# Optimization experiments

Measured on AMD Instinct MI355X. Metric: run time of the kernel, lower is better.

## Reference

```python
import jax, jax.numpy as jnp
import numpy as np

N, E, Z, C, B, G, T = 10000, 160000, 10, 64, 8, 16, 2
R_MAX = 5.0
AVG_NEIGH = 16.0
L_SLICES = ((0, 1), (1, 4), (4, 9))  # l=0,1,2 blocks of the 9 SH components


def sph_harm(u):
    # component-normalized real spherical harmonics up to l=2, u: [E,3] unit vectors
    x, y, z = u[:, 0], u[:, 1], u[:, 2]
    s3, s5, s15 = 3.0 ** 0.5, 5.0 ** 0.5, 15.0 ** 0.5
    return jnp.stack([
        jnp.ones_like(x),
        s3 * x, s3 * y, s3 * z,
        s15 * x * y, s15 * y * z, (s5 / 2) * (3 * z * z - 1), s15 * x * z, (s15 / 2) * (x * x - y * y),
    ], axis=1)  # [E,9]


def radial_embed(r):
    # Bessel basis * polynomial cutoff (p=5), r: [E]
    u = r / R_MAX
    n = jnp.arange(1, B + 1, dtype=jnp.float32)
    bessel = jnp.sqrt(2.0 / R_MAX) * jnp.sin(n[None, :] * jnp.pi * u[:, None]) / (r[:, None] + 1e-9)
    p = 5.0
    fc = 1 - (p + 1) * (p + 2) / 2 * u ** p + p * (p + 2) * u ** (p + 1) - p * (p + 1) / 2 * u ** (p + 2)
    fc = jnp.where(u < 1.0, fc, 0.0)
    return bessel * fc[:, None]  # [E,B]


def per_l_linear(x, W):
    # x: [n,C,9], W: [3,C,C]; independent channel mixing per l-block
    return jnp.concatenate([
        jnp.einsum('ncm,cd->ndm', x[:, :, s:e], W[l]) for l, (s, e) in enumerate(L_SLICES)
    ], axis=2)


def _forward(positions, node_attrs, charges, shifts, W_emb, atomic_energies,
             W_r1, W_r2, W_mix, W_sc, w_poly, W_prod, w_e, w_d,
             edge_index, batch, num_graphs):
    sender, receiver = edge_index[0], edge_index[1]
    # atomic reference energies
    node_e0 = node_attrs @ atomic_energies  # [N]
    e0 = jax.ops.segment_sum(node_e0, batch, num_segments=num_graphs)
    # node embedding: scalars only
    node_feats = jnp.zeros((positions.shape[0], C, 9), positions.dtype)
    node_feats = node_feats.at[:, :, 0].set(node_attrs @ W_emb)
    # edge geometry
    vec = positions[sender] - positions[receiver] + shifts  # [E,3]
    lengths = jnp.sqrt(jnp.sum(vec * vec, axis=1) + 1e-12)
    sh = sph_harm(vec / lengths[:, None])        # [E,9]
    edge_feats = radial_embed(lengths)           # [E,B]
    energies = [e0]
    dipoles = []
    for t in range(T):
        # radial MLP -> per-channel TP weights
        w = jax.nn.silu(edge_feats @ W_r1[t]) @ W_r2[t]      # [E,C]
        h_s = node_feats[sender, :, 0]                       # gather sender scalars [E,C]
        m = (w * h_s)[:, :, None] * sh[:, None, :]           # TP message [E,C,9]
        agg = jax.ops.segment_sum(m, receiver, num_segments=positions.shape[0]) / AVG_NEIGH
        msg = per_l_linear(agg, W_mix[t])
        sc = per_l_linear(node_feats, W_sc[t])               # self-connection
        # product basis (correlation 3): channel-wise scalar polynomial gate
        s0 = msg[:, :, 0]
        poly = w_poly[t, :, 0][None] + w_poly[t, :, 1][None] * s0 + w_poly[t, :, 2][None] * s0 * s0
        node_feats = per_l_linear(msg * poly[:, :, None], W_prod[t]) + sc
        # readout: 1x0e energy + 1x1o dipole
        e_n = node_feats[:, :, 0] @ w_e[t]                   # [N]
        energies.append(jax.ops.segment_sum(e_n, batch, num_segments=num_graphs))
        dipoles.append(jnp.einsum('ncm,c->nm', node_feats[:, :, 1:4], w_d[t]))  # [N,3]
    contributions = jnp.stack(energies, axis=-1)             # [G,T+1]
    total_energy = jnp.sum(contributions, axis=-1)           # [G]
    atomic_dipoles = jnp.sum(jnp.stack(dipoles, axis=-1), axis=-1)  # [N,3]
    total_dipole = jax.ops.segment_sum(atomic_dipoles, batch, num_segments=num_graphs)
    total_dipole = total_dipole + jax.ops.segment_sum(charges[:, None] * positions, batch, num_segments=num_graphs)
    return total_energy, contributions, atomic_dipoles, total_dipole


def setup_inputs():
    key = jax.random.key(0)
    ks = jax.random.split(key, 16)
    s = 0.1
    species = jax.random.randint(ks[1], (N,), 0, Z)
    return {
        'positions': jax.random.normal(ks[0], (N, 3)) * 3.0,
        'node_attrs': jax.nn.one_hot(species, Z, dtype=jnp.float32),
        'charges': jax.random.normal(ks[2], (N,)) * 0.1,
        'shifts': jnp.zeros((E, 3), jnp.float32),
        'W_emb': jax.random.normal(ks[5], (Z, C)) * s,
        'atomic_energies': jax.random.normal(ks[6], (Z,)) * s,
        'W_r1': jax.random.normal(ks[7], (T, B, 64)) * s,
        'W_r2': jax.random.normal(ks[8], (T, 64, C)) * s,
        'W_mix': jax.random.normal(ks[9], (T, 3, C, C)) * s,
        'W_sc': jax.random.normal(ks[10], (T, 3, C, C)) * s,
        'w_poly': jax.random.normal(ks[11], (T, C, 3)) * s,
        'W_prod': jax.random.normal(ks[12], (T, 3, C, C)) * s,
        'w_e': jax.random.normal(ks[13], (T, C)) * s,
        'w_d': jax.random.normal(ks[14], (T, C)) * s,
        'edge_index': jax.random.randint(ks[3], (2, E), 0, N),
        'batch': jnp.sort(jax.random.randint(ks[4], (N,), 0, G)),
        'num_graphs': G,
    }


def reference(positions, node_attrs, charges, shifts, W_emb, atomic_energies,
              W_r1, W_r2, W_mix, W_sc, w_poly, W_prod, w_e, w_d,
              edge_index, batch, num_graphs):
    args = (node_attrs, charges, shifts, W_emb, atomic_energies, W_r1, W_r2,
            W_mix, W_sc, w_poly, W_prod, w_e, w_d, edge_index, batch, num_graphs)
    total_energy, contributions, atomic_dipoles, total_dipole = _forward(positions, *args)
    forces = -jax.grad(lambda p: jnp.sum(_forward(p, *args)[0]))(positions)
    return total_energy, contributions, forces, total_dipole, atomic_dipoles
```

## Files before the change

### kernel.cpp

```cpp
#include <hip/hip_runtime.h>
#include <hip/hip_bf16.h>

#define NN 10000
#define NE 160000
#define NZ 10
#define NBES 8
#define NG 16
#define NT 2
#define NB 2048
#define NB1 2049
#define PL ((size_t)NN*64)

static constexpr float PI_F  = 3.14159265358979323846f;
static constexpr float KBES  = 0.63245553203367587f;
static constexpr float S3    = 1.73205080756887729f;

static constexpr size_t OFF_UVL  = 0;
static constexpr size_t OFF_PIN  = OFF_UVL + (size_t)NE*4;
static constexpr size_t OFF_ATT  = OFF_PIN + (size_t)NN*3;
static constexpr size_t OFF_CHG  = OFF_ATT + (size_t)NN*NZ;
static constexpr size_t OFF_SHF  = OFF_CHG + (size_t)NN;
static constexpr size_t OFF_NF0  = OFF_SHF + (size_t)NE*3;
static constexpr size_t OFF_NF1  = OFF_NF0 + PL;
static constexpr size_t OFF_MSG0 = OFF_NF1 + 4*PL;
static constexpr size_t OFF_MSG1 = OFF_MSG0 + 4*PL;
static constexpr size_t OFF_AGG  = OFF_MSG1 + 4*PL;
static constexpr size_t O_GA1    = OFF_MSG0 + PL;
static constexpr size_t O_GA0    = OFF_AGG;
static constexpr size_t OFF_W    = OFF_AGG + 4*PL;
static constexpr size_t O_WEMB   = OFF_W;
static constexpr size_t O_AE     = O_WEMB + 640;
static constexpr size_t O_R1     = O_AE   + 16;
static constexpr size_t O_R2     = O_R1   + 1024;
static constexpr size_t O_WMIX   = O_R2   + 8192;
static constexpr size_t O_WMIXT  = O_WMIX + 24576;
static constexpr size_t O_WSC    = O_WMIXT+ 24576;
static constexpr size_t O_WSCT   = O_WSC  + 24576;
static constexpr size_t O_WPROD  = O_WSCT + 24576;
static constexpr size_t O_WPRODT = O_WPROD+ 24576;
static constexpr size_t O_WPOLY  = O_WPRODT+24576;
static constexpr size_t O_WE     = O_WPOLY+ 384;
static constexpr size_t O_WD     = O_WE   + 128;
static constexpr size_t OFF_ACC  = O_WD   + 128;
static constexpr size_t O_E0G    = OFF_ACC;
static constexpr size_t O_ETG    = O_E0G + 16;
static constexpr size_t O_TD     = O_ETG + 32;
static constexpr size_t O_ADP    = O_TD  + 48;
static constexpr size_t O_GPOS   = O_ADP + (size_t)NN*3;
static constexpr size_t ACC_FLOATS = 96 + (size_t)NN*6;
static constexpr size_t O_EN0    = O_GPOS + (size_t)NN*3;
static constexpr size_t O_EN1    = O_EN0 + NN;
static constexpr size_t O_E0N    = O_EN1 + NN;
static constexpr size_t O_FLAG   = O_E0N + NN;
static constexpr size_t O_TW     = O_FLAG + 4;
static constexpr size_t O_TQ     = O_TW + (size_t)2*NB1*64;
static constexpr size_t O_OFFR   = O_TQ + (size_t)2*NB1*64;
static constexpr size_t O_OFFS   = O_OFFR + (NN+1);
static constexpr size_t O_CURR   = O_OFFS + (NN+1);
static constexpr size_t O_CURS   = O_CURR + NN;
static constexpr size_t O_RECRAW = O_CURS + NN;
static constexpr size_t O_RECR   = (O_RECRAW + 7) & ~(size_t)7;
static constexpr size_t O_RECS   = O_RECR + (size_t)NE*8 + 64;
static constexpr size_t WS_FLOATS= O_RECS + (size_t)NE*8 + 64;

__device__ __forceinline__ float rlane(float v, int l){
  return __int_as_float(__builtin_amdgcn_readlane(__float_as_int(v), l));
}
__device__ __forceinline__ int irlane(float v, int l){
  return __builtin_amdgcn_readlane(__float_as_int(v), l);
}

static constexpr int LD_CNT[14] = {NN*3, NN*NZ, NN, NE*3, NZ*64, NZ, NT*NBES*64, NT*64*64,
                                   NT*3*64*64, NT*3*64*64, NT*64*3, NT*3*64*64, NT*64, NT*64};
static constexpr int LD_TOTAL = NN*3 + NN*NZ + NN + NE*3 + NZ*64 + NZ + NT*NBES*64 + NT*64*64
                              + 3*(NT*3*64*64) + NT*64*3 + 4*(NT*64) - NT*64*2;
__global__ __launch_bounds__(256) void k_load_all(
    const void* s0, const void* s1, const void* s2, const void* s3, const void* s4,
    const void* s5, const void* s6, const void* s7, const void* s8, const void* s9,
    const void* s10, const void* s11, const void* s12, const void* s13,
    float* __restrict__ ws){
  __shared__ int found;
  if (threadIdx.x == 0) found = 0;
  __syncthreads();
  const unsigned* raw = (const unsigned*)s1;
  int f = 0;
  for (int i = threadIdx.x; i < 4096; i += 256){
    unsigned w = raw[i];
    f |= (w == 0x00003F80u || w == 0x3F803F80u) ? 1 : 0;
  }
  if (f) found = 1;
  __syncthreads();
  const int isbf = found;
  if (blockIdx.x == 0 && threadIdx.x == 0) ((int*)(ws + O_FLAG))[0] = isbf;

  const void* srcs[14] = {s0,s1,s2,s3,s4,s5,s6,s7,s8,s9,s10,s11,s12,s13};
  const size_t dsts[14] = {OFF_PIN, OFF_ATT, OFF_CHG, OFF_SHF, O_WEMB, O_AE, O_R1, O_R2,
                           O_WMIX, O_WSC, O_WPOLY, O_WPROD, O_WE, O_WD};
  int i = blockIdx.x*256 + threadIdx.x;
  int seg = -1, off = i;
  #pragma unroll
  for (int j = 0; j < 14; ++j){
    if (seg < 0){
      if (off < LD_CNT[j]) seg = j;
      else off -= LD_CNT[j];
    }
  }
  if (seg < 0) return;
  float v = isbf ? __bfloat162float(((const __hip_bfloat16*)srcs[seg])[off])
                 : ((const float*)srcs[seg])[off];
  ws[dsts[seg] + off] = v;
}

static constexpr int GEOM_B = (NE+255)/256;
static constexpr int TAB_B  = (2*NB1+3)/4;
static constexpr int INIT_B = (NN+3)/4;
static constexpr int TRAN_B = 5*4096/256;
__global__ __launch_bounds__(256, 3) void k_prep(float* __restrict__ ws, const int* __restrict__ ei){
  int b = blockIdx.x;
  if (b < GEOM_B){
    int e = b*256 + threadIdx.x;
    if (e >= NE) return;
    const float* pos = ws + OFF_PIN;
    const float* shifts = ws + OFF_SHF;
    int s = ei[e], r = ei[NE + e];
    float vx = pos[s*3+0] - pos[r*3+0] + shifts[(size_t)e*3+0];
    float vy = pos[s*3+1] - pos[r*3+1] + shifts[(size_t)e*3+1];
    float vz = pos[s*3+2] - pos[r*3+2] + shifts[(size_t)e*3+2];
    float L = sqrtf(vx*vx + vy*vy + vz*vz + 1e-12f);
    float inv = 1.f / L;
    float4 uq; uq.x = vx*inv; uq.y = vy*inv; uq.z = vz*inv; uq.w = L;
    *(float4*)(ws + OFF_UVL + (size_t)e*4) = uq;
    if (L < 5.f){
      atomicAdd((int*)(ws + O_CURR) + r, 1);
      atomicAdd((int*)(ws + O_CURS) + s, 1);
    }
  } else if (b < GEOM_B + TAB_B){
    int lane = threadIdx.x & 63;
    int task = (b - GEOM_B)*4 + (threadIdx.x >> 6);
    if (task >= 2*NB1) return;
    int t = task / NB1, node = task % NB1;
    const float* R1 = ws + O_R1 + (size_t)t*512;
    const float* R2 = ws + O_R2 + (size_t)t*4096;
    float r1c[8];
    #pragma unroll
    for (int j = 0; j < 8; ++j) r1c[j] = R1[j*64 + lane];
    float L = fmaxf((float)node * (5.f/NB), 1e-6f);
    float ur = L*0.2f;
    float ef[8], dd[8];
    if (ur < 1.f){
      float u2=ur*ur, u4=u2*u2, u5=u4*ur;
      float fc = 1.f - 21.f*u5 + 35.f*u5*ur - 15.f*u5*u2;
      float omu = 1.f - ur;
      float dfc = -105.f*u4*omu*omu;
      float invr = 1.f/(L + 1e-9f);
      #pragma unroll
      for (int bb = 0; bb < 8; ++bb){
        float nb = (float)(bb+1);
        float arg = nb*PI_F*ur;
        float sn = __sinf(arg), cs = __cosf(arg);
        float bes = KBES*sn*invr;
        float dbes = KBES*(nb*PI_F*0.2f)*cs*invr - bes*invr;
        ef[bb] = bes*fc;
        dd[bb] = dbes*fc + bes*dfc*0.2f;
      }
    } else {
      #pragma unroll
      for (int bb = 0; bb < 8; ++bb){ ef[bb] = 0.f; dd[bb] = 0.f; }
    }
    float a = 0.f, tt = 0.f;
    #pragma unroll
    for (int bb = 0; bb < 8; ++bb){ a = fmaf(ef[bb], r1c[bb], a); tt = fmaf(r1c[bb], dd[bb], tt); }
    float sg = 1.f/(1.f + __expf(-a));
    float sl = a*sg;
    float q  = sg*fmaf(a, 1.f - sg, 1.f)*tt;
    float r2c[64];
    #pragma unroll
    for (int j = 0; j < 64; ++j) r2c[j] = R2[j*64 + lane];
    float W0=0.f, W1=0.f, Q0=0.f, Q1=0.f;
    #pragma unroll
    for (int j = 0; j < 64; j += 2){
      W0 = fmaf(rlane(sl, j  ), r2c[j  ], W0);
      W1 = fmaf(rlane(sl, j+1), r2c[j+1], W1);
      Q0 = fmaf(rlane(q,  j  ), r2c[j  ], Q0);
      Q1 = fmaf(rlane(q,  j+1), r2c[j+1], Q1);
    }
    size_t idx = ((size_t)t*NB1 + node)*64 + lane;
    ws[O_TW + idx] = (W0+W1)*(1.f/16.f);
    ws[O_TQ + idx] = (Q0+Q1)*(1.f/16.f);
  } else if (b < GEOM_B + TAB_B + INIT_B){
    int lane = threadIdx.x & 63;
    int n = (b - GEOM_B - TAB_B)*4 + (threadIdx.x >> 6);
    if (n >= NN) return;
    const float* attrs = ws + OFF_ATT;
    float acc = 0.f;
    #pragma unroll
    for (int z = 0; z < NZ; ++z) acc = fmaf(attrs[(size_t)n*NZ+z], ws[O_WEMB + z*64 + lane], acc);
    ws[OFF_NF0 + (size_t)n*64 + lane] = acc;
    if (lane == 0){
      float e = 0.f;
      #pragma unroll
      for (int z = 0; z < NZ; ++z) e = fmaf(attrs[(size_t)n*NZ+z], ws[O_AE + z], e);
      ws[O_E0N + n] = e;
    }
  } else {
    int i = (b - GEOM_B - TAB_B - INIT_B)*256 + threadIdx.x;
    int mat = i >> 12, r = (i >> 6) & 63, c = i & 63;
    const size_t src[5] = {O_WMIX, O_WMIX+12288, O_WPROD, O_WPROD+12288, O_WSC+12288};
    const size_t dst[5] = {O_WMIXT, O_WMIXT+12288, O_WPRODT, O_WPRODT+12288, O_WSCT+12288};
    ws[dst[mat] + (size_t)c*64 + r] = ws[src[mat] + (size_t)r*64 + c];
  }
}

__global__ __launch_bounds__(1024) void k_csr_scan(
    int* __restrict__ curr, int* __restrict__ curs,
    int* __restrict__ offr, int* __restrict__ offs_){
  __shared__ unsigned short cr[NN], cs[NN];
  __shared__ int pr[1024], ps[1024];
  int tid = threadIdx.x;
  for (int i = tid; i < NN; i += 1024){
    cr[i] = (unsigned short)curr[i];
    cs[i] = (unsigned short)curs[i];
  }
  __syncthreads();
  const int chunk = (NN + 1023)/1024;
  int lo = tid*chunk, hi = lo + chunk;
  if (hi > NN) hi = NN;
  if (lo > NN) lo = NN;
  int sr = 0, ss = 0;
  for (int i = lo; i < hi; ++i){ sr += cr[i]; ss += cs[i]; }
  pr[tid] = sr; ps[tid] = ss;
  __syncthreads();
  for (int o = 1; o < 1024; o <<= 1){
    int vr = (tid >= o) ? pr[tid-o] : 0;
    int vs = (tid >= o) ? ps[tid-o] : 0;
    __syncthreads();
    pr[tid] += vr; ps[tid] += vs;
    __syncthreads();
  }
  int runr = tid ? pr[tid-1] : 0;
  int runs = tid ? ps[tid-1] : 0;
  for (int i = lo; i < hi; ++i){
    int a = cr[i], c = cs[i];
    offr[i] = runr; curr[i] = runr; runr += a;
    offs_[i] = runs; curs[i] = runs; runs += c;
  }
  if (tid == 1023){ offr[NN] = runr; offs_[NN] = runs; }
}

__global__ void k_csr_fill(const int* __restrict__ ei, const float* __restrict__ uvl,
                           int* __restrict__ curr, int* __restrict__ curs,
                           float* __restrict__ recr, float* __restrict__ recs){
  int e = blockIdx.x*256 + threadIdx.x;
  if (e >= NE) return;
  float4 q = *(const float4*)(uvl + (size_t)e*4);
  if (q.w >= 5.f) return;
  int s = ei[e], r = ei[NE + e];
  int4 meta; meta.x = s; meta.y = r; meta.z = e; meta.w = 0;
  int pr = atomicAdd(&curr[r], 1);
  *(float4*)(recr + (size_t)pr*8) = q;
  *(int4*)(recr + (size_t)pr*8 + 4) = meta;
  int ps = atomicAdd(&curs[s], 1);
  *(float4*)(recs + (size_t)ps*8) = q;
  *(int4*)(recs + (size_t)ps*8 + 4) = meta;
}

__global__ __launch_bounds__(256) void k_agg(
    const float* __restrict__ TWt, const float* __restrict__ recr,
    const float* __restrict__ h, const int* __restrict__ offr,
    float* __restrict__ agg){
  int lane = threadIdx.x & 63;
  int wid = blockIdx.x*4 + (threadIdx.x >> 6);
  int nw  = gridDim.x*4;
  for (int n = wid; n < NN; n += nw){
    int lo = offr[n], hi = offr[n+1];
    float c0=0.f, x1=0.f, y1=0.f, z1=0.f;
    for (int i = lo; i < hi; i += 8){
      float rv = recr[(size_t)i*8 + lane];
      int cnt = hi - i;
      if (cnt >= 8){
        #pragma unroll
        for (int j = 0; j < 8; ++j){
          float ux = rlane(rv, j*8+0), uy = rlane(rv, j*8+1), uz = rlane(rv, j*8+2);
          float L  = rlane(rv, j*8+3);
          int   s  = irlane(rv, j*8+4);
          float pos = L*(NB/5.f); int bi = (int)pos; float f = pos - (float)bi;
          const float* T = TWt + (size_t)bi*64 + lane;
          float t0 = T[0];
          float w = fmaf(T[64]-t0, f, t0);
          float wh = w * h[(size_t)s*64 + lane];
          c0 += wh;
          x1 = fmaf(wh, ux, x1);
          y1 = fmaf(wh, uy, y1);
          z1 = fmaf(wh, uz, z1);
        }
      } else {
        for (int j = 0; j < cnt; ++j){
          float ux = rlane(rv, j*8+0), uy = rlane(rv, j*8+1), uz = rlane(rv, j*8+2);
          float L  = rlane(rv, j*8+3);
          int   s  = irlane(rv, j*8+4);
          float pos = L*(NB/5.f); int bi = (int)pos; float f = pos - (float)bi;
          const float* T = TWt + (size_t)bi*64 + lane;
          float t0 = T[0];
          float w = fmaf(T[64]-t0, f, t0);
          float wh = w * h[(size_t)s*64 + lane];
          c0 += wh;
          x1 = fmaf(wh, ux, x1);
          y1 = fmaf(wh, uy, y1);
          z1 = fmaf(wh, uz, z1);
        }
      }
    }
    size_t ob = (size_t)n*64 + lane;
    agg[ob]        = c0;
    agg[ob+PL]     = S3*x1;
    agg[ob+2*PL]   = S3*y1;
    agg[ob+3*PL]   = S3*z1;
  }
}

template<int GB1>
__global__ __launch_bounds__(256, 3) void k_lin2(
    const float* __restrict__ in, const float* __restrict__ W3, float* __restrict__ out,
    const float* __restrict__ WMIXT1, const float* __restrict__ WPRODT1,
    const float* __restrict__ we1, const float* __restrict__ wp1,
    float* __restrict__ ga1){
  int k = blockIdx.y;
  int l = (k==0) ? 0 : 1;
  const float* W = W3 + (size_t)l*4096;
  int lane = threadIdx.x & 63;
  float wcol[64];
  #pragma unroll
  for (int j = 0; j < 64; ++j) wcol[j] = W[j*64 + lane];
  float wcol2[64];
  float g = 0.f, p0 = 0.f, p1 = 0.f, p2 = 0.f;
  const bool gb1 = GB1 && (k == 0);
  if (gb1){
    #pragma unroll
    for (int j = 0; j < 64; ++j) wcol2[j] = WMIXT1[j*64 + lane];
    #pragma unroll
    for (int c = 0; c < 64; ++c) g = fmaf(we1[c], WPRODT1[c*64 + lane], g);
    p0 = wp1[lane*3]; p1 = wp1[lane*3+1]; p2 = wp1[lane*3+2];
  }
  int wid = blockIdx.x*4 + (threadIdx.x >> 6);
  int nw  = gridDim.x*4;
  const float* inp = in + (size_t)k*PL;
  float* outp = out + (size_t)k*PL;
  for (int n = wid; n < NN; n += nw){
    float x = inp[(size_t)n*64 + lane];
    float a0 = 0.f, a1 = 0.f, a2 = 0.f, a3 = 0.f;
    #pragma unroll
    for (int j = 0; j < 64; j += 4){
      a0 = fmaf(rlane(x, j  ), wcol[j  ], a0);
      a1 = fmaf(rlane(x, j+1), wcol[j+1], a1);
      a2 = fmaf(rlane(x, j+2), wcol[j+2], a2);
      a3 = fmaf(rlane(x, j+3), wcol[j+3], a3);
    }
    float m = (a0+a1) + (a2+a3);
    outp[(size_t)n*64 + lane] = m;
    if (gb1){
      float poly = fmaf(fmaf(p2, m, p1), m, p0);
      float dp   = fmaf(2.f*p2, m, p1);
      float gb = g*fmaf(m, dp, poly);
      float b0=0.f, b1=0.f, b2=0.f, b3=0.f;
      #pragma unroll
      for (int j = 0; j < 64; j += 4){
        b0 = fmaf(rlane(gb, j  ), wcol2[j  ], b0);
        b1 = fmaf(rlane(gb, j+1), wcol2[j+1], b1);
        b2 = fmaf(rlane(gb, j+2), wcol2[j+2], b2);
        b3 = fmaf(rlane(gb, j+3), wcol2[j+3], b3);
      }
      ga1[(size_t)n*64 + lane] = (b0+b1) + (b2+b3);
    }
  }
}

template<int WRITE_NF, int NF_SINGLE>
__global__ __launch_bounds__(256, 3) void k_tail(
    const float* __restrict__ nf_in, const float* __restrict__ msg,
    const float* __restrict__ Wsc, const float* __restrict__ Wprod, const float* __restrict__ wp,
    const float* __restrict__ we, const float* __restrict__ wd,
    float* __restrict__ nf_out, float* __restrict__ en, float* __restrict__ adp){
  int lane = threadIdx.x & 63;
  int k = threadIdx.x >> 6;
  int l = (k==0) ? 0 : 1;
  const bool use_sc = !(NF_SINGLE && k > 0);
  float wcs[64], wcp[64];
  #pragma unroll
  for (int j = 0; j < 64; ++j)
    wcp[j] = Wprod[(size_t)l*4096 + j*64 + lane];
  if (use_sc){
    #pragma unroll
    for (int j = 0; j < 64; ++j)
      wcs[j] = Wsc[(size_t)l*4096 + j*64 + lane];
  }
  float p0 = wp[lane*3], p1 = wp[lane*3+1], p2 = wp[lane*3+2];
  float rw = (k==0) ? we[lane] : wd[lane];
  const float* msgk = msg + (size_t)k*PL;
  const float* nfk  = nf_in + (size_t)k*PL;
  float* outk = nf_out + (size_t)k*PL;
  for (int n = blockIdx.x; n < NN; n += gridDim.x){
    size_t base = (size_t)n*64 + lane;
    float s0 = msg[base];
    float xm = (k==0) ? s0 : msgk[base];
    float xg = xm * fmaf(fmaf(p2, s0, p1), s0, p0);
    float b0=0.f, b1=0.f;
    #pragma unroll
    for (int j = 0; j < 64; j += 2){
      b0 = fmaf(rlane(xg, j  ), wcp[j  ], b0);
      b1 = fmaf(rlane(xg, j+1), wcp[j+1], b1);
    }
    float out = b0 + b1;
    if (use_sc){
      float xs = nfk[base];
      float a0=0.f, a1=0.f;
      #pragma unroll
      for (int j = 0; j < 64; j += 2){
        a0 = fmaf(rlane(xs, j  ), wcs[j  ], a0);
        a1 = fmaf(rlane(xs, j+1), wcs[j+1], a1);
      }
      out += a0 + a1;
    }
    if (WRITE_NF) outk[base] = out;
    float red = out * rw;
    #pragma unroll
    for (int o = 32; o; o >>= 1) red += __shfl_xor(red, o, 64);
    if (lane == 0){
      if (k == 0) en[n] = red;
      else        adp[n*3 + (k-1)] += red;
    }
  }
}

static constexpr int GHG_GRID = 1024;
static constexpr int RED_B = (NN+255)/256;
__global__ __launch_bounds__(256) void k_ghg0(float* __restrict__ ws, const int* __restrict__ offs_,
                                              const int* __restrict__ batch){
  __shared__ float wl[2*4096];
  if (blockIdx.x >= GHG_GRID){
    int n = (blockIdx.x - GHG_GRID)*256 + threadIdx.x;
    int lane = threadIdx.x & 63;
    bool valid = (n < NN);
    int g = valid ? batch[n] : -1;
    float v0=0.f, v1=0.f, v2=0.f, tx=0.f, ty=0.f, tz=0.f;
    if (valid){
      v0 = ws[O_E0N + n]; v1 = ws[O_EN0 + n]; v2 = ws[O_EN1 + n];
      float qq = ws[OFF_CHG + n];
      tx = ws[O_ADP + n*3+0] + qq*ws[OFF_PIN + n*3+0];
      ty = ws[O_ADP + n*3+1] + qq*ws[OFF_PIN + n*3+1];
      tz = ws[O_ADP + n*3+2] + qq*ws[OFF_PIN + n*3+2];
    }
    float* e0g = ws + O_E0G; float* Etg = ws + O_ETG; float* td = ws + O_TD;
    int g0 = __shfl(g, 0, 64), g63 = __shfl(g, 63, 64);
    if (g0 == g63 && g0 >= 0){
      #pragma unroll
      for (int o = 32; o; o >>= 1){
        v0 += __shfl_xor(v0, o, 64); v1 += __shfl_xor(v1, o, 64); v2 += __shfl_xor(v2, o, 64);
        tx += __shfl_xor(tx, o, 64); ty += __shfl_xor(ty, o, 64); tz += __shfl_xor(tz, o, 64);
      }
      if (lane == 0){
        atomicAdd(&e0g[g0], v0); atomicAdd(&Etg[g0], v1); atomicAdd(&Etg[16+g0], v2);
        atomicAdd(&td[g0*3+0], tx); atomicAdd(&td[g0*3+1], ty); atomicAdd(&td[g0*3+2], tz);
      }
    } else if (valid){
      atomicAdd(&e0g[g], v0); atomicAdd(&Etg[g], v1); atomicAdd(&Etg[16+g], v2);
      atomicAdd(&td[g*3+0], tx); atomicAdd(&td[g*3+1], ty); atomicAdd(&td[g*3+2], tz);
    }
    return;
  }
  for (int i = threadIdx.x; i < 4096; i += 256){
    wl[i]        = ws[O_WPRODT + i];
    wl[4096 + i] = ws[O_WMIXT + i];
  }
  __syncthreads();
  const int lane = threadIdx.x & 63;
  int wid = blockIdx.x*4 + (threadIdx.x >> 6);
  const int nw = GHG_GRID*4;
  float gnfc = ws[O_WE + lane];
  {
    const float* WS1 = ws + O_WSCT + 12288;
    const float* we1 = ws + O_WE + 64;
    #pragma unroll
    for (int c = 0; c < 64; ++c) gnfc = fmaf(we1[c], WS1[c*64 + lane], gnfc);
  }
  const float p0 = ws[O_WPOLY + lane*3];
  const float p1 = ws[O_WPOLY + lane*3 + 1];
  const float p2 = ws[O_WPOLY + lane*3 + 2];
  const float* TW1 = ws + O_TW + (size_t)NB1*64;
  const float* recs = ws + O_RECS;
  const float* GA1 = ws + O_GA1;
  for (int n = wid; n < NN; n += nw){
    int lo = offs_[n], hi = offs_[n+1];
    float acc = 0.f;
    for (int i = lo; i < hi; i += 8){
      float rv = recs[(size_t)i*8 + lane];
      int cnt = hi - i;
      if (cnt >= 8){
        #pragma unroll
        for (int j = 0; j < 8; ++j){
          float L = rlane(rv, j*8+3);
          int   r = irlane(rv, j*8+5);
          float pos = L*(NB/5.f); int bi = (int)pos; float f = pos - (float)bi;
          const float* T = TW1 + (size_t)bi*64 + lane;
          float t0 = T[0];
          float w = fmaf(T[64]-t0, f, t0);
          acc = fmaf(w, GA1[(size_t)r*64 + lane], acc);
        }
      } else {
        for (int j = 0; j < cnt; ++j){
          float L = rlane(rv, j*8+3);
          int   r = irlane(rv, j*8+5);
          float pos = L*(NB/5.f); int bi = (int)pos; float f = pos - (float)bi;
          const float* T = TW1 + (size_t)bi*64 + lane;
          float t0 = T[0];
          float w = fmaf(T[64]-t0, f, t0);
          acc = fmaf(w, GA1[(size_t)r*64 + lane], acc);
        }
      }
    }
    float gB = gnfc + acc;
    float q0=0.f, q1=0.f;
    #pragma unroll
    for (int j = 0; j < 64; j += 2){
      q0 = fmaf(rlane(gB,j),   wl[j*64 + lane],     q0);
      q1 = fmaf(rlane(gB,j+1), wl[(j+1)*64 + lane], q1);
    }
    float gmp = q0 + q1;
    float s0v = ws[OFF_MSG0 + (size_t)n*64 + lane];
    float poly = fmaf(fmaf(p2, s0v, p1), s0v, p0);
    float dp   = fmaf(2.f*p2, s0v, p1);
    float gb = gmp * fmaf(s0v, dp, poly);
    float u0=0.f, u1=0.f;
    #pragma unroll
    for (int j = 0; j < 64; j += 2){
      u0 = fmaf(rlane(gb,j),   wl[4096 + j*64 + lane],     u0);
      u1 = fmaf(rlane(gb,j+1), wl[4096 + (j+1)*64 + lane], u1);
    }
    ws[O_GA0 + (size_t)n*64 + lane] = u0 + u1;
  }
}

__global__ __launch_bounds__(256) void k_bwdE2(float* __restrict__ ws, const int* __restrict__ nlive_ptr){
  const int lane = threadIdx.x & 63;
  int wid = blockIdx.x*4 + (threadIdx.x >> 6);
  const int nw = gridDim.x*4;
  const int nlive = nlive_ptr[0];
  const int ngrp = (nlive + 7) >> 3;
  const float* recs = ws + O_RECS;
  const float* TQ  = ws + O_TQ;
  const float* h0  = ws + OFF_NF0;
  const float* h1  = ws + OFF_NF1;
  const float* ga0 = ws + O_GA0;
  const float* ga1 = ws + O_GA1;
  float* gpos = ws + O_GPOS;
  for (int gi = wid; gi < ngrp; gi += nw){
    const int i0 = gi*8;
    float rv = recs[(size_t)i0*8 + lane];
    int cnt = nlive - i0; if (cnt > 8) cnt = 8;
    #pragma unroll 8
    for (int j = 0; j < cnt; ++j){
      float ux = rlane(rv, j*8+0), uy = rlane(rv, j*8+1), uz = rlane(rv, j*8+2);
      float L  = rlane(rv, j*8+3);
      int   s  = irlane(rv, j*8+4);
      int   r  = irlane(rv, j*8+5);
      float pos = L*(NB/5.f); int bi = (int)pos; float f = pos - (float)bi;
      const float* T0 = TQ + (size_t)bi*64 + lane;
      const float* T1 = T0 + (size_t)NB1*64;
      float Q0 = fmaf(T0[64]-T0[0], f, T0[0]);
      float Q1 = fmaf(T1[64]-T1[0], f, T1[0]);
      float rr = Q0*h0[(size_t)s*64 + lane]*ga0[(size_t)r*64 + lane]
               + Q1*h1[(size_t)s*64 + lane]*ga1[(size_t)r*64 + lane];
      #pragma unroll
      for (int o = 32; o; o >>= 1) rr += __shfl_xor(rr, o, 64);
      if (lane < 3){
        float u = (lane==0) ? ux : ((lane==1) ? uy : uz);
        float v = rr*u;
        atomicAdd(&gpos[(size_t)s*3 + lane],  v);
        atomicAdd(&gpos[(size_t)r*3 + lane], -v);
      }
    }
  }
}

__global__ void k_writeout(const float* __restrict__ e0g, const float* __restrict__ Etg,
                           const float* __restrict__ td, const float* __restrict__ adp,
                           const float* __restrict__ gpos, void* __restrict__ outv,
                           const int* __restrict__ flag){
  int i = blockIdx.x*256 + threadIdx.x;
  const int total = NG + NG*3 + NN*3 + NG*3 + NN*3;
  if (i >= total) return;
  float v;
  if (i < 16){
    v = e0g[i] + Etg[i] + Etg[16+i];
  } else if (i < 64){
    int j = i - 16; int g = j/3, t = j - g*3;
    v = (t == 0) ? e0g[g] : Etg[(t-1)*16 + g];
  } else if (i < 64 + NN*3){
    v = -gpos[i-64];
  } else if (i < 64 + NN*3 + 48){
    v = td[i - (64 + NN*3)];
  } else {
    v = adp[i - (64 + NN*3 + 48)];
  }
  if (flag[0]) ((__hip_bfloat16*)outv)[i] = __float2bfloat16(v);
  else         ((float*)outv)[i] = v;
}

extern "C" void kernel_launch(void* const* d_in, const int* in_sizes, int n_in,
                              void* d_out, int out_size, void* d_ws, size_t ws_size,
                              hipStream_t stream) {
  if (ws_size < WS_FLOATS*sizeof(float)) return;
  const int* ei    = (const int*)d_in[14];
  const int* batch = (const int*)d_in[15];
  float* ws = (float*)d_ws;

  int* offr  = (int*)(ws + O_OFFR);
  int* offs_ = (int*)(ws + O_OFFS);
  int* curr  = (int*)(ws + O_CURR);
  int* curs  = (int*)(ws + O_CURS);

  hipMemsetAsync(ws + OFF_ACC, 0, ACC_FLOATS*sizeof(float), stream);
  hipMemsetAsync(curr, 0, 2*NN*sizeof(int), stream);

  k_load_all<<<(LD_TOTAL+255)/256, 256, 0, stream>>>(
      d_in[0], d_in[1], d_in[2], d_in[3], d_in[4], d_in[5], d_in[6], d_in[7],
      d_in[8], d_in[9], d_in[10], d_in[11], d_in[12], d_in[13], ws);
  k_prep<<<GEOM_B + TAB_B + INIT_B + TRAN_B, 256, 0, stream>>>(ws, ei);
  k_csr_scan<<<1, 1024, 0, stream>>>(curr, curs, offr, offs_);
  k_csr_fill<<<(NE+255)/256, 256, 0, stream>>>(ei, ws+OFF_UVL, curr, curs,
                                               ws+O_RECR, ws+O_RECS);

  dim3 ling(256, 4);

  k_agg<<<1024, 256, 0, stream>>>(ws+O_TW, ws+O_RECR, ws+OFF_NF0, offr, ws+OFF_AGG);
  k_lin2<0><<<ling, 256, 0, stream>>>(ws+OFF_AGG, ws+O_WMIX, ws+OFF_MSG0,
                                      ws, ws, ws, ws, ws);
  k_tail<1,1><<<1024, 256, 0, stream>>>(ws+OFF_NF0, ws+OFF_MSG0,
                                        ws+O_WSC, ws+O_WPROD,
                                        ws+O_WPOLY, ws+O_WE, ws+O_WD,
                                        ws+OFF_NF1, ws+O_EN0, ws+O_ADP);
  k_agg<<<1024, 256, 0, stream>>>(ws+O_TW + (size_t)NB1*64, ws+O_RECR, ws+OFF_NF1, offr, ws+OFF_AGG);
  k_lin2<1><<<ling, 256, 0, stream>>>(ws+OFF_AGG, ws+O_WMIX + 12288, ws+OFF_MSG1,
                                      ws+O_WMIXT + 12288, ws+O_WPRODT + 12288,
                                      ws+O_WE + 64, ws+O_WPOLY + 192, ws+O_GA1);
  k_tail<0,0><<<1024, 256, 0, stream>>>(ws+OFF_NF1, ws+OFF_MSG1,
                                        ws+O_WSC + 12288, ws+O_WPROD + 12288,
                                        ws+O_WPOLY + 192, ws+O_WE + 64, ws+O_WD + 64,
                                        ws+OFF_NF1, ws+O_EN1, ws+O_ADP);

  k_ghg0<<<GHG_GRID + RED_B, 256, 0, stream>>>(ws, offs_, batch);
  k_bwdE2<<<2048, 256, 0, stream>>>(ws, offs_ + NN);

  k_writeout<<<(60112+255)/256, 256, 0, stream>>>(ws+O_E0G, ws+O_ETG, ws+O_TD, ws+O_ADP,
                                                  ws+O_GPOS, d_out, (const int*)(ws+O_FLAG));
}
```

Measured before the change: 332.4 us.

## Interleave radial table neighbors as float2, prefetch edge records, move weights to registers

The radial weight tables are stored interleaved so each lane fetches both interpolation endpoints in a single float2 load, where before it issued two separate scalar loads. The edge-record loops in k_agg and k_ghg0 now prefetch the next group of 8 records while the current group is processed. k_ghg0 keeps its two 64x64 weight columns in registers instead of shared memory, and launch bounds are added to several kernels. In exchange the tables take twice the memory and register pressure rises, which could cause spills or lower occupancy.

```diff
diff --git a/kernel.cpp b/kernel.cpp
--- a/kernel.cpp
+++ b/kernel.cpp
@@ -53,8 +53,8 @@
 static constexpr size_t O_E0N    = O_EN1 + NN;
 static constexpr size_t O_FLAG   = O_E0N + NN;
 static constexpr size_t O_TW     = O_FLAG + 4;
-static constexpr size_t O_TQ     = O_TW + (size_t)2*NB1*64;
-static constexpr size_t O_OFFR   = O_TQ + (size_t)2*NB1*64;
+static constexpr size_t O_TQ     = O_TW + (size_t)2*NB1*128;
+static constexpr size_t O_OFFR   = O_TQ + (size_t)2*NB1*128;
 static constexpr size_t O_OFFS   = O_OFFR + (NN+1);
 static constexpr size_t O_CURR   = O_OFFS + (NN+1);
 static constexpr size_t O_CURS   = O_CURR + NN;
@@ -184,9 +184,15 @@
       Q0 = fmaf(rlane(q,  j  ), r2c[j  ], Q0);
       Q1 = fmaf(rlane(q,  j+1), r2c[j+1], Q1);
     }
-    size_t idx = ((size_t)t*NB1 + node)*64 + lane;
-    ws[O_TW + idx] = (W0+W1)*(1.f/16.f);
-    ws[O_TQ + idx] = (Q0+Q1)*(1.f/16.f);
+    float Wv = (W0+W1)*(1.f/16.f);
+    float Qv = (Q0+Q1)*(1.f/16.f);
+    size_t base2 = ((size_t)t*NB1 + node)*128 + (size_t)lane*2;
+    ws[O_TW + base2] = Wv;
+    ws[O_TQ + base2] = Qv;
+    if (node > 0){
+      ws[O_TW + base2 - 128 + 1] = Wv;
+      ws[O_TQ + base2 - 128 + 1] = Qv;
+    }
   } else if (b < GEOM_B + TAB_B + INIT_B){
     int lane = threadIdx.x & 63;
     int n = (b - GEOM_B - TAB_B)*4 + (threadIdx.x >> 6);
@@ -264,7 +270,7 @@
   *(int4*)(recs + (size_t)ps*8 + 4) = meta;
 }
 
-__global__ __launch_bounds__(256) void k_agg(
+__global__ __launch_bounds__(256, 4) void k_agg(
     const float* __restrict__ TWt, const float* __restrict__ recr,
     const float* __restrict__ h, const int* __restrict__ offr,
     float* __restrict__ agg){
@@ -274,40 +280,43 @@
   for (int n = wid; n < NN; n += nw){
     int lo = offr[n], hi = offr[n+1];
     float c0=0.f, x1=0.f, y1=0.f, z1=0.f;
-    for (int i = lo; i < hi; i += 8){
-      float rv = recr[(size_t)i*8 + lane];
-      int cnt = hi - i;
-      if (cnt >= 8){
-        #pragma unroll
-        for (int j = 0; j < 8; ++j){
-          float ux = rlane(rv, j*8+0), uy = rlane(rv, j*8+1), uz = rlane(rv, j*8+2);
-          float L  = rlane(rv, j*8+3);
-          int   s  = irlane(rv, j*8+4);
-          float pos = L*(NB/5.f); int bi = (int)pos; float f = pos - (float)bi;
-          const float* T = TWt + (size_t)bi*64 + lane;
-          float t0 = T[0];
-          float w = fmaf(T[64]-t0, f, t0);
-          float wh = w * h[(size_t)s*64 + lane];
-          c0 += wh;
-          x1 = fmaf(wh, ux, x1);
-          y1 = fmaf(wh, uy, y1);
-          z1 = fmaf(wh, uz, z1);
+    if (lo < hi){
+      float rv = recr[(size_t)lo*8 + lane];
+      for (int i = lo; i < hi; ){
+        int ni = i + 8;
+        float rvn = (ni < hi) ? recr[(size_t)ni*8 + lane] : 0.f;
+        int cnt = hi - i;
+        if (cnt >= 8){
+          #pragma unroll
+          for (int j = 0; j < 8; ++j){
+            float ux = rlane(rv, j*8+0), uy = rlane(rv, j*8+1), uz = rlane(rv, j*8+2);
+            float L  = rlane(rv, j*8+3);
+            int   s  = irlane(rv, j*8+4);
+            float pos = L*(NB/5.f); int bi = (int)pos; float f = pos - (float)bi;
+            const float2 tp = *(const float2*)(TWt + ((size_t)bi*64 + lane)*2);
+            float w = fmaf(tp.y - tp.x, f, tp.x);
+            float wh = w * h[(size_t)s*64 + lane];
+            c0 += wh;
+            x1 = fmaf(wh, ux, x1);
+            y1 = fmaf(wh, uy, y1);
+            z1 = fmaf(wh, uz, z1);
+          }
+        } else {
+          for (int j = 0; j < cnt; ++j){
+            float ux = rlane(rv, j*8+0), uy = rlane(rv, j*8+1), uz = rlane(rv, j*8+2);
+            float L  = rlane(rv, j*8+3);
+            int   s  = irlane(rv, j*8+4);
+            float pos = L*(NB/5.f); int bi = (int)pos; float f = pos - (float)bi;
+            const float2 tp = *(const float2*)(TWt + ((size_t)bi*64 + lane)*2);
+            float w = fmaf(tp.y - tp.x, f, tp.x);
+            float wh = w * h[(size_t)s*64 + lane];
+            c0 += wh;
+            x1 = fmaf(wh, ux, x1);
+            y1 = fmaf(wh, uy, y1);
+            z1 = fmaf(wh, uz, z1);
+          }
         }
-      } else {
-        for (int j = 0; j < cnt; ++j){
-          float ux = rlane(rv, j*8+0), uy = rlane(rv, j*8+1), uz = rlane(rv, j*8+2);
-          float L  = rlane(rv, j*8+3);
-          int   s  = irlane(rv, j*8+4);
-          float pos = L*(NB/5.f); int bi = (int)pos; float f = pos - (float)bi;
-          const float* T = TWt + (size_t)bi*64 + lane;
-          float t0 = T[0];
-          float w = fmaf(T[64]-t0, f, t0);
-          float wh = w * h[(size_t)s*64 + lane];
-          c0 += wh;
-          x1 = fmaf(wh, ux, x1);
-          y1 = fmaf(wh, uy, y1);
-          z1 = fmaf(wh, uz, z1);
-        }
+        rv = rvn; i = ni;
       }
     }
     size_t ob = (size_t)n*64 + lane;
@@ -433,9 +442,8 @@
 
 static constexpr int GHG_GRID = 1024;
 static constexpr int RED_B = (NN+255)/256;
-__global__ __launch_bounds__(256) void k_ghg0(float* __restrict__ ws, const int* __restrict__ offs_,
-                                              const int* __restrict__ batch){
-  __shared__ float wl[2*4096];
+__global__ __launch_bounds__(256, 2) void k_ghg0(float* __restrict__ ws, const int* __restrict__ offs_,
+                                                 const int* __restrict__ batch){
   if (blockIdx.x >= GHG_GRID){
     int n = (blockIdx.x - GHG_GRID)*256 + threadIdx.x;
     int lane = threadIdx.x & 63;
@@ -467,12 +475,12 @@
     }
     return;
   }
-  for (int i = threadIdx.x; i < 4096; i += 256){
-    wl[i]        = ws[O_WPRODT + i];
-    wl[4096 + i] = ws[O_WMIXT + i];
-  }
-  __syncthreads();
   const int lane = threadIdx.x & 63;
+  float wcp[64], wcm[64];
+  #pragma unroll
+  for (int j = 0; j < 64; ++j) wcp[j] = ws[O_WPRODT + j*64 + lane];
+  #pragma unroll
+  for (int j = 0; j < 64; ++j) wcm[j] = ws[O_WMIXT + j*64 + lane];
   int wid = blockIdx.x*4 + (threadIdx.x >> 6);
   const int nw = GHG_GRID*4;
   float gnfc = ws[O_WE + lane];
@@ -485,44 +493,47 @@
   const float p0 = ws[O_WPOLY + lane*3];
   const float p1 = ws[O_WPOLY + lane*3 + 1];
   const float p2 = ws[O_WPOLY + lane*3 + 2];
-  const float* TW1 = ws + O_TW + (size_t)NB1*64;
+  const float* TW1 = ws + O_TW + (size_t)NB1*128;
   const float* recs = ws + O_RECS;
   const float* GA1 = ws + O_GA1;
   for (int n = wid; n < NN; n += nw){
     int lo = offs_[n], hi = offs_[n+1];
     float acc = 0.f;
-    for (int i = lo; i < hi; i += 8){
-      float rv = recs[(size_t)i*8 + lane];
-      int cnt = hi - i;
-      if (cnt >= 8){
-        #pragma unroll
-        for (int j = 0; j < 8; ++j){
-          float L = rlane(rv, j*8+3);
-          int   r = irlane(rv, j*8+5);
-          float pos = L*(NB/5.f); int bi = (int)pos; float f = pos - (float)bi;
-          const float* T = TW1 + (size_t)bi*64 + lane;
-          float t0 = T[0];
-          float w = fmaf(T[64]-t0, f, t0);
-          acc = fmaf(w, GA1[(size_t)r*64 + lane], acc);
+    if (lo < hi){
+      float rv = recs[(size_t)lo*8 + lane];
+      for (int i = lo; i < hi; ){
+        int ni = i + 8;
+        float rvn = (ni < hi) ? recs[(size_t)ni*8 + lane] : 0.f;
+        int cnt = hi - i;
+        if (cnt >= 8){
+          #pragma unroll
+          for (int j = 0; j < 8; ++j){
+            float L = rlane(rv, j*8+3);
+            int   r = irlane(rv, j*8+5);
+            float pos = L*(NB/5.f); int bi = (int)pos; float f = pos - (float)bi;
+            const float2 tp = *(const float2*)(TW1 + ((size_t)bi*64 + lane)*2);
+            float w = fmaf(tp.y - tp.x, f, tp.x);
+            acc = fmaf(w, GA1[(size_t)r*64 + lane], acc);
+          }
+        } else {
+          for (int j = 0; j < cnt; ++j){
+            float L = rlane(rv, j*8+3);
+            int   r = irlane(rv, j*8+5);
+            float pos = L*(NB/5.f); int bi = (int)pos; float f = pos - (float)bi;
+            const float2 tp = *(const float2*)(TW1 + ((size_t)bi*64 + lane)*2);
+            float w = fmaf(tp.y - tp.x, f, tp.x);
+            acc = fmaf(w, GA1[(size_t)r*64 + lane], acc);
+          }
         }
-      } else {
-        for (int j = 0; j < cnt; ++j){
-          float L = rlane(rv, j*8+3);
-          int   r = irlane(rv, j*8+5);
-          float pos = L*(NB/5.f); int bi = (int)pos; float f = pos - (float)bi;
-          const float* T = TW1 + (size_t)bi*64 + lane;
-          float t0 = T[0];
-          float w = fmaf(T[64]-t0, f, t0);
-          acc = fmaf(w, GA1[(size_t)r*64 + lane], acc);
-        }
+        rv = rvn; i = ni;
       }
     }
     float gB = gnfc + acc;
     float q0=0.f, q1=0.f;
     #pragma unroll
     for (int j = 0; j < 64; j += 2){
-      q0 = fmaf(rlane(gB,j),   wl[j*64 + lane],     q0);
-      q1 = fmaf(rlane(gB,j+1), wl[(j+1)*64 + lane], q1);
+      q0 = fmaf(rlane(gB,j),   wcp[j  ], q0);
+      q1 = fmaf(rlane(gB,j+1), wcp[j+1], q1);
     }
     float gmp = q0 + q1;
     float s0v = ws[OFF_MSG0 + (size_t)n*64 + lane];
@@ -532,21 +543,22 @@
     float u0=0.f, u1=0.f;
     #pragma unroll
     for (int j = 0; j < 64; j += 2){
-      u0 = fmaf(rlane(gb,j),   wl[4096 + j*64 + lane],     u0);
-      u1 = fmaf(rlane(gb,j+1), wl[4096 + (j+1)*64 + lane], u1);
+      u0 = fmaf(rlane(gb,j),   wcm[j  ], u0);
+      u1 = fmaf(rlane(gb,j+1), wcm[j+1], u1);
     }
     ws[O_GA0 + (size_t)n*64 + lane] = u0 + u1;
   }
 }
 
-__global__ __launch_bounds__(256) void k_bwdE2(float* __restrict__ ws, const int* __restrict__ nlive_ptr){
+__global__ __launch_bounds__(256, 4) void k_bwdE2(float* __restrict__ ws, const int* __restrict__ nlive_ptr){
   const int lane = threadIdx.x & 63;
   int wid = blockIdx.x*4 + (threadIdx.x >> 6);
   const int nw = gridDim.x*4;
   const int nlive = nlive_ptr[0];
   const int ngrp = (nlive + 7) >> 3;
   const float* recs = ws + O_RECS;
-  const float* TQ  = ws + O_TQ;
+  const float* TQ0 = ws + O_TQ;
+  const float* TQ1 = ws + O_TQ + (size_t)NB1*128;
   const float* h0  = ws + OFF_NF0;
   const float* h1  = ws + OFF_NF1;
   const float* ga0 = ws + O_GA0;
@@ -563,10 +575,10 @@
       int   s  = irlane(rv, j*8+4);
       int   r  = irlane(rv, j*8+5);
       float pos = L*(NB/5.f); int bi = (int)pos; float f = pos - (float)bi;
-      const float* T0 = TQ + (size_t)bi*64 + lane;
-      const float* T1 = T0 + (size_t)NB1*64;
-      float Q0 = fmaf(T0[64]-T0[0], f, T0[0]);
-      float Q1 = fmaf(T1[64]-T1[0], f, T1[0]);
+      const float2 t0 = *(const float2*)(TQ0 + ((size_t)bi*64 + lane)*2);
+      const float2 t1 = *(const float2*)(TQ1 + ((size_t)bi*64 + lane)*2);
+      float Q0 = fmaf(t0.y - t0.x, f, t0.x);
+      float Q1 = fmaf(t1.y - t1.x, f, t1.x);
       float rr = Q0*h0[(size_t)s*64 + lane]*ga0[(size_t)r*64 + lane]
                + Q1*h1[(size_t)s*64 + lane]*ga1[(size_t)r*64 + lane];
       #pragma unroll
@@ -638,7 +650,7 @@
                                         ws+O_WSC, ws+O_WPROD,
                                         ws+O_WPOLY, ws+O_WE, ws+O_WD,
                                         ws+OFF_NF1, ws+O_EN0, ws+O_ADP);
-  k_agg<<<1024, 256, 0, stream>>>(ws+O_TW + (size_t)NB1*64, ws+O_RECR, ws+OFF_NF1, offr, ws+OFF_AGG);
+  k_agg<<<1024, 256, 0, stream>>>(ws+O_TW + (size_t)NB1*128, ws+O_RECR, ws+OFF_NF1, offr, ws+OFF_AGG);
   k_lin2<1><<<ling, 256, 0, stream>>>(ws+OFF_AGG, ws+O_WMIX + 12288, ws+OFF_MSG1,
                                       ws+O_WMIXT + 12288, ws+O_WPRODT + 12288,
                                       ws+O_WE + 64, ws+O_WPOLY + 192, ws+O_GA1);
```

Measured after the change: 335.0 us. Within noise of the previous version (+0.8%).

## Move layer-1 edge position-gradient term into k_ghg0 as extra blocks

Applied to the files above, without the earlier changes.

The layer-1 contribution to the edge force accumulation (using h1, ga1 and the second radial table) is split out of k_bwdE2 and computed by extra blocks appended to the k_ghg0 launch. This lets it overlap with the ghg0 work, since it depends only on data that is ready before that kernel, and it shortens the k_bwdE2 critical path. In exchange the edge records are read twice and the atomics to gpos are doubled, which adds memory traffic and atomic contention.

```diff
diff --git a/kernel.cpp b/kernel.cpp
--- a/kernel.cpp
+++ b/kernel.cpp
@@ -433,9 +433,47 @@
 
 static constexpr int GHG_GRID = 1024;
 static constexpr int RED_B = (NN+255)/256;
+static constexpr int EDGE1_B = 1024;
 __global__ __launch_bounds__(256) void k_ghg0(float* __restrict__ ws, const int* __restrict__ offs_,
                                               const int* __restrict__ batch){
   __shared__ float wl[2*4096];
+  if (blockIdx.x >= GHG_GRID + RED_B){
+    const int lane = threadIdx.x & 63;
+    int wid = (blockIdx.x - GHG_GRID - RED_B)*4 + (threadIdx.x >> 6);
+    const int nw = EDGE1_B*4;
+    const int nlive = offs_[NN];
+    const int ngrp = (nlive + 7) >> 3;
+    const float* recs = ws + O_RECS;
+    const float* TQ1 = ws + O_TQ + (size_t)NB1*64;
+    const float* h1  = ws + OFF_NF1;
+    const float* ga1 = ws + O_GA1;
+    float* gpos = ws + O_GPOS;
+    for (int gi = wid; gi < ngrp; gi += nw){
+      const int i0 = gi*8;
+      float rv = recs[(size_t)i0*8 + lane];
+      int cnt = nlive - i0; if (cnt > 8) cnt = 8;
+      #pragma unroll 8
+      for (int j = 0; j < cnt; ++j){
+        float ux = rlane(rv, j*8+0), uy = rlane(rv, j*8+1), uz = rlane(rv, j*8+2);
+        float L  = rlane(rv, j*8+3);
+        int   s  = irlane(rv, j*8+4);
+        int   r  = irlane(rv, j*8+5);
+        float pos = L*(NB/5.f); int bi = (int)pos; float f = pos - (float)bi;
+        const float* T1 = TQ1 + (size_t)bi*64 + lane;
+        float Q1 = fmaf(T1[64]-T1[0], f, T1[0]);
+        float rr = Q1*h1[(size_t)s*64 + lane]*ga1[(size_t)r*64 + lane];
+        #pragma unroll
+        for (int o = 32; o; o >>= 1) rr += __shfl_xor(rr, o, 64);
+        if (lane < 3){
+          float u = (lane==0) ? ux : ((lane==1) ? uy : uz);
+          float v = rr*u;
+          atomicAdd(&gpos[(size_t)s*3 + lane],  v);
+          atomicAdd(&gpos[(size_t)r*3 + lane], -v);
+        }
+      }
+    }
+    return;
+  }
   if (blockIdx.x >= GHG_GRID){
     int n = (blockIdx.x - GHG_GRID)*256 + threadIdx.x;
     int lane = threadIdx.x & 63;
@@ -548,9 +586,7 @@
   const float* recs = ws + O_RECS;
   const float* TQ  = ws + O_TQ;
   const float* h0  = ws + OFF_NF0;
-  const float* h1  = ws + OFF_NF1;
   const float* ga0 = ws + O_GA0;
-  const float* ga1 = ws + O_GA1;
   float* gpos = ws + O_GPOS;
   for (int gi = wid; gi < ngrp; gi += nw){
     const int i0 = gi*8;
@@ -564,11 +600,8 @@
       int   r  = irlane(rv, j*8+5);
       float pos = L*(NB/5.f); int bi = (int)pos; float f = pos - (float)bi;
       const float* T0 = TQ + (size_t)bi*64 + lane;
-      const float* T1 = T0 + (size_t)NB1*64;
       float Q0 = fmaf(T0[64]-T0[0], f, T0[0]);
-      float Q1 = fmaf(T1[64]-T1[0], f, T1[0]);
-      float rr = Q0*h0[(size_t)s*64 + lane]*ga0[(size_t)r*64 + lane]
-               + Q1*h1[(size_t)s*64 + lane]*ga1[(size_t)r*64 + lane];
+      float rr = Q0*h0[(size_t)s*64 + lane]*ga0[(size_t)r*64 + lane];
       #pragma unroll
       for (int o = 32; o; o >>= 1) rr += __shfl_xor(rr, o, 64);
       if (lane < 3){
@@ -647,7 +680,7 @@
                                         ws+O_WPOLY + 192, ws+O_WE + 64, ws+O_WD + 64,
                                         ws+OFF_NF1, ws+O_EN1, ws+O_ADP);
 
-  k_ghg0<<<GHG_GRID + RED_B, 256, 0, stream>>>(ws, offs_, batch);
+  k_ghg0<<<GHG_GRID + RED_B + EDGE1_B, 256, 0, stream>>>(ws, offs_, batch);
   k_bwdE2<<<2048, 256, 0, stream>>>(ws, offs_ + NN);
 
   k_writeout<<<(60112+255)/256, 256, 0, stream>>>(ws+O_E0G, ws+O_ETG, ws+O_TD, ws+O_ADP,
```

Measured after the change: 342.4 us. +3.0%, slower.
